# Optimization experiments

Measured on AMD Instinct MI355X. Metric: run time of the kernel, lower is better.

## Reference

```python
import jax, jax.numpy as jnp
import numpy as np

B, L, D_MODEL = 4, 4096, 1024
D_STATE, D_CONV, N_HEADS, CHUNK = 16, 4, 8, 64
D_INNER = 2048
HEADDIM = D_INNER // N_HEADS
CONV_DIM = D_INNER + 2 * D_STATE
D_PROJ = 2 * D_INNER + 2 * D_STATE + N_HEADS
EPS = 1e-5


def _silu(v):
    return v * jax.nn.sigmoid(v)


def _segsum(x):
    # x: (..., T) -> (..., T, T); segsum[i,j] = sum_{j<d<=i} x[d], -inf above diag
    T = x.shape[-1]
    xe = jnp.broadcast_to(x[..., None], (*x.shape, T))
    lower_strict = jnp.tril(jnp.ones((T, T), bool), -1)
    s = jnp.cumsum(jnp.where(lower_strict, xe, 0.0), axis=-2)
    lower = jnp.tril(jnp.ones((T, T), bool), 0)
    return jnp.where(lower, s, -jnp.inf)


def _ssd(x, A, Bm, Cm, chunk):
    # x: (b,l,h,p), A: (b,l,h), Bm/Cm: (b,l,n) (single B/C shared across heads)
    b, l, h, p = x.shape
    n = Bm.shape[-1]
    c = l // chunk
    x = x.reshape(b, c, chunk, h, p)
    A = A.reshape(b, c, chunk, h).transpose(0, 3, 1, 2)  # b h c l
    Bc = Bm.reshape(b, c, chunk, n)
    Cc = Cm.reshape(b, c, chunk, n)
    A_cs = jnp.cumsum(A, axis=-1)                        # b h c l
    Lmat = jnp.exp(_segsum(A))                           # b h c l s
    Y_diag = jnp.einsum('bcln,bcsn,bhcls,bcshp->bclhp', Cc, Bc, Lmat, x)
    decay_states = jnp.exp(A_cs[..., -1:] - A_cs)        # b h c l
    states = jnp.einsum('bcln,bhcl,bclhp->bchpn', Bc, decay_states, x)
    states = jnp.concatenate([jnp.zeros_like(states[:, :1]), states], axis=1)
    A_last = jnp.pad(A_cs[..., -1], ((0, 0), (0, 0), (1, 0)))  # b h (c+1)
    decay_chunk = jnp.exp(_segsum(A_last))               # b h (c+1) (c+1)
    new_states = jnp.einsum('bhzc,bchpn->bzhpn', decay_chunk, states)
    states_prev, final_state = new_states[:, :-1], new_states[:, -1]
    Y_off = jnp.einsum('bcln,bchpn,bhcl->bclhp', Cc, states_prev, jnp.exp(A_cs))
    Y = (Y_diag + Y_off).reshape(b, l, h, p)
    return Y, final_state


def setup_inputs() -> dict:
    key = jax.random.key(0)
    ks = jax.random.split(key, 8)
    inp = {
        'input_tensor': jax.random.normal(ks[0], (B, L, D_MODEL), dtype=jnp.float32),
        'W_in': jax.random.normal(ks[1], (D_PROJ, D_MODEL), dtype=jnp.float32) / np.sqrt(D_MODEL),
        'conv_w': jax.random.normal(ks[2], (CONV_DIM, 1, D_CONV), dtype=jnp.float32) * 0.2,
        'conv_b': jax.random.normal(ks[3], (CONV_DIM,), dtype=jnp.float32) * 0.02,
        'dt_bias': jax.random.uniform(ks[4], (N_HEADS,), dtype=jnp.float32) * 0.1,
        'log_A': jnp.log(jnp.arange(1, N_HEADS + 1, dtype=jnp.float32)),
        'D_skip': jnp.ones((N_HEADS,), dtype=jnp.float32),
        'norm_w': jnp.ones((D_INNER,), dtype=jnp.float32),
        'W_out': jax.random.normal(ks[5], (D_MODEL, D_INNER), dtype=jnp.float32) / np.sqrt(D_INNER),
    }
    return inp


def reference(input_tensor, W_in, conv_w, conv_b, dt_bias, log_A, D_skip, norm_w, W_out):
    bsz, slen, _ = input_tensor.shape
    proj = input_tensor @ W_in.T  # (b,l,D_PROJ)
    z = proj[..., :D_INNER]
    xBC = proj[..., D_INNER:D_INNER + CONV_DIM]
    dt = jax.nn.softplus(proj[..., D_INNER + CONV_DIM:] + dt_bias)  # (b,l,h)
    # causal depthwise conv1d (torch pads both sides then slices [:, :slen])
    xt = jnp.transpose(xBC, (0, 2, 1))  # (b,d,l)
    conv = jax.lax.conv_general_dilated(
        xt, conv_w, window_strides=(1,), padding=[(D_CONV - 1, 0)],
        feature_group_count=CONV_DIM) + conv_b[None, :, None]
    xBC = _silu(jnp.transpose(conv, (0, 2, 1)))
    x = xBC[..., :D_INNER]
    Bm = xBC[..., D_INNER:D_INNER + D_STATE]
    Cm = xBC[..., D_INNER + D_STATE:]
    A = jnp.broadcast_to((-jnp.exp(log_A))[None, None, :], (bsz, slen, N_HEADS))
    xh = x.reshape(bsz, slen, N_HEADS, HEADDIM) * dt[..., None]
    Y, _ = _ssd(xh, A, Bm, Cm, CHUNK)
    Y = Y + xh * D_skip[:, None]
    y = Y.reshape(bsz, slen, D_INNER)
    # gated RMSNorm
    y = y * _silu(z)
    y = y * jax.lax.rsqrt(jnp.mean(y * y, axis=-1, keepdims=True) + EPS) * norm_w
    return y @ W_out.T
```

## Files before the change

kernel.cpp:

```cpp
#include <hip/hip_runtime.h>
#include <hip/hip_bf16.h>
#include <math.h>

#define BATCH   4
#define SEQLEN  4096
#define DMODEL  1024
#define DSTATE  16
#define DCONV   4
#define NHEADS  8
#define CHUNKSZ 64
#define DINNER  2048
#define HEADDIM 256
#define CONVDIM 2080
#define DPROJ   4136
#define NPAD1   4224
#define LDP     4224
#define ROWS    (BATCH*SEQLEN)
#define NCHUNK  (SEQLEN/CHUNKSZ)

typedef unsigned short bf16_t;
typedef __attribute__((ext_vector_type(8))) short bfrag;
typedef __attribute__((ext_vector_type(4))) float f32x4;

__device__ __forceinline__ float sigmoidf_(float v) { return 1.0f / (1.0f + __expf(-v)); }
__device__ __forceinline__ float siluf_(float v)    { return v * sigmoidf_(v); }
__device__ __forceinline__ float softplusf_(float v) {
    return fmaxf(v, 0.f) + log1pf(__expf(-fabsf(v)));
}

__device__ __forceinline__ float bf2f(bf16_t u) {
    union { unsigned int i; float f; } v; v.i = ((unsigned int)u) << 16; return v.f;
}
__device__ __forceinline__ float bflo(unsigned int u) {
    union { unsigned int i; float f; } v; v.i = u << 16; return v.f;
}
__device__ __forceinline__ float bfhi(unsigned int u) {
    union { unsigned int i; float f; } v; v.i = u & 0xffff0000u; return v.f;
}
__device__ __forceinline__ bf16_t f2bf(float f) {
    unsigned int x = __float_as_uint(f);
    unsigned int r = (x + 0x7fffu + ((x >> 16) & 1u)) >> 16;
    return (bf16_t)r;
}
__device__ __forceinline__ unsigned int pack2(float a, float b) {
    return (unsigned int)f2bf(a) | ((unsigned int)f2bf(b) << 16);
}

__device__ __forceinline__ void async_copy16(const bf16_t* g, bf16_t* l) {
    __builtin_amdgcn_global_load_lds(
        (const __attribute__((address_space(1))) void*)g,
        (__attribute__((address_space(3))) void*)l, 16, 0, 0);
}

__global__ __launch_bounds__(256)
void cvt_f32_bf16(const float* __restrict__ src, bf16_t* __restrict__ dst, int n8)
{
    int i = blockIdx.x * 256 + threadIdx.x;
    if (i >= n8) return;
    float4 a = *(const float4*)&src[(size_t)i * 8];
    float4 b = *(const float4*)&src[(size_t)i * 8 + 4];
    uint4 o;
    o.x = pack2(a.x, a.y); o.y = pack2(a.z, a.w);
    o.z = pack2(b.x, b.y); o.w = pack2(b.z, b.w);
    *(uint4*)&dst[(size_t)i * 8] = o;
}

__global__ __launch_bounds__(256)
void cvt_pad_w1(const float* __restrict__ src, bf16_t* __restrict__ dst)
{
    int i = blockIdx.x * 256 + threadIdx.x;
    if (i >= NPAD1 * DMODEL / 4) return;
    size_t e = (size_t)i * 4;
    int row = (int)(e >> 10);
    ushort4 o = make_ushort4(0, 0, 0, 0);
    if (row < DPROJ) {
        float4 v = *(const float4*)&src[e];
        o.x = f2bf(v.x); o.y = f2bf(v.y); o.z = f2bf(v.z); o.w = f2bf(v.w);
    }
    *(ushort4*)&dst[e] = o;
}

__global__ __launch_bounds__(256)
void cvt_w2(const float* __restrict__ W, const float* __restrict__ norm_w,
            bf16_t* __restrict__ dst)
{
    int i = blockIdx.x * 256 + threadIdx.x;
    if (i >= DMODEL * DINNER / 4) return;
    size_t e = (size_t)i * 4;
    int k = (int)(e & (DINNER - 1));
    float4 v = *(const float4*)&W[e];
    float4 w = *(const float4*)&norm_w[k];
    ushort4 o;
    o.x = f2bf(v.x * w.x); o.y = f2bf(v.y * w.y);
    o.z = f2bf(v.z * w.z); o.w = f2bf(v.w * w.w);
    *(ushort4*)&dst[e] = o;
}

template<bool OUT_BF16>
__device__ __forceinline__
void gemm_body(const bf16_t* __restrict__ A, const bf16_t* __restrict__ W,
               void* __restrict__ Cv, const float* __restrict__ rowScale,
               int Nstore, int K, int lda, int ldw, int ldc)
{
    __shared__ __align__(16) bf16_t smem[16384];
    bf16_t* As = smem;
    bf16_t* Ws = smem + 8192;
    const int tid  = threadIdx.x;
    const int wave = tid >> 6, lane = tid & 63;
    const int row0 = blockIdx.y * 128, col0 = blockIdx.x * 128;
    const int wm = (wave >> 1) * 64, wn = (wave & 1) * 64;
    const int quad = lane >> 4, fr = lane & 15;

    const int sr  = lane >> 2;
    const int cph = lane & 3;
    const int r1  = wave * 32 + sr;
    const int cl1 = cph ^ ((r1 >> 1) & 3);
    const bf16_t* gA1 = &A[(size_t)(row0 + r1) * lda + cl1 * 8];
    const bf16_t* gW1 = &W[(size_t)(col0 + r1) * ldw + cl1 * 8];
    const size_t offA16 = (size_t)16 * lda;
    const size_t offW16 = (size_t)16 * ldw;
    const int lo1 = wave * 1024, lo2 = wave * 1024 + 512;

    int aoff[4], boff[4];
    #pragma unroll
    for (int i = 0; i < 4; ++i) {
        int ar = wm + i * 16 + fr;
        aoff[i] = ar * 32 + ((quad ^ ((ar >> 1) & 3)) << 3);
        int br = wn + i * 16 + fr;
        boff[i] = br * 32 + ((quad ^ ((br >> 1) & 3)) << 3);
    }

    f32x4 acc[4][4];
    #pragma unroll
    for (int i = 0; i < 4; ++i)
        #pragma unroll
        for (int j = 0; j < 4; ++j) {
            f32x4 z = {0.f, 0.f, 0.f, 0.f};
            acc[i][j] = z;
        }

    const int niter = K >> 5;
    async_copy16(gA1, &As[lo1]);
    async_copy16(gA1 + offA16, &As[lo2]);
    async_copy16(gW1, &Ws[lo1]);
    async_copy16(gW1 + offW16, &Ws[lo2]);

    for (int it = 0; it < niter; ++it) {
        const int cur = (it & 1) * 4096;
        __syncthreads();
        if (it + 1 < niter) {
            const int nxt = cur ^ 4096;
            const int kt = (it + 1) * 32;
            async_copy16(gA1 + kt, &As[nxt + lo1]);
            async_copy16(gA1 + kt + offA16, &As[nxt + lo2]);
            async_copy16(gW1 + kt, &Ws[nxt + lo1]);
            async_copy16(gW1 + kt + offW16, &Ws[nxt + lo2]);
        }
        bfrag af[4], bfr[4];
        #pragma unroll
        for (int i = 0; i < 4; ++i) af[i]  = *(const bfrag*)&As[cur + aoff[i]];
        #pragma unroll
        for (int j = 0; j < 4; ++j) bfr[j] = *(const bfrag*)&Ws[cur + boff[j]];
        #pragma unroll
        for (int i = 0; i < 4; ++i)
            #pragma unroll
            for (int j = 0; j < 4; ++j)
                acc[i][j] = __builtin_amdgcn_mfma_f32_16x16x32_bf16(
                                af[i], bfr[j], acc[i][j], 0, 0, 0);
    }

    float rs[4][4];
    if (rowScale) {
        #pragma unroll
        for (int i = 0; i < 4; ++i) {
            size_t m = (size_t)row0 + wm + i * 16 + quad * 4;
            #pragma unroll
            for (int r = 0; r < 4; ++r) rs[i][r] = rowScale[m + r];
        }
    } else {
        #pragma unroll
        for (int i = 0; i < 4; ++i)
            #pragma unroll
            for (int r = 0; r < 4; ++r) rs[i][r] = 1.f;
    }

    if (OUT_BF16) {
        __syncthreads();
        bf16_t* C = (bf16_t*)Cv;
        #pragma unroll
        for (int pass = 0; pass < 2; ++pass) {
            if ((wave >> 1) == pass) {
                #pragma unroll
                for (int i = 0; i < 4; ++i)
                    #pragma unroll
                    for (int j = 0; j < 4; ++j) {
                        int col = wn + 16 * j + fr;
                        #pragma unroll
                        for (int r = 0; r < 4; ++r) {
                            int rl = 16 * i + quad * 4 + r;
                            smem[rl * 136 + col] = f2bf(acc[i][j][r] * rs[i][r]);
                        }
                    }
            }
            __syncthreads();
            #pragma unroll
            for (int k = 0; k < 4; ++k) {
                int id = k * 256 + tid;
                int rl = id >> 4, ch = id & 15;
                uint4 v = *(const uint4*)&smem[rl * 136 + ch * 8];
                *(uint4*)&C[(size_t)(row0 + pass * 64 + rl) * ldc + col0 + ch * 8] = v;
            }
            if (pass == 0) __syncthreads();
        }
    } else {
        float* C = (float*)Cv;
        #pragma unroll
        for (int j = 0; j < 4; ++j) {
            int n = col0 + wn + j * 16 + fr;
            if (n < Nstore) {
                #pragma unroll
                for (int i = 0; i < 4; ++i) {
                    size_t m = (size_t)row0 + wm + i * 16 + quad * 4;
                    #pragma unroll
                    for (int r = 0; r < 4; ++r)
                        C[(m + r) * ldc + n] = acc[i][j][r] * rs[i][r];
                }
            }
        }
    }
}

__global__ __launch_bounds__(256)
void gemm_g1(const bf16_t* __restrict__ A, const bf16_t* __restrict__ W,
             void* __restrict__ Cv, const float* __restrict__ rowScale,
             int Nstore, int K, int lda, int ldw, int ldc)
{ gemm_body<true>(A, W, Cv, rowScale, Nstore, K, lda, ldw, ldc); }

__global__ __launch_bounds__(256)
void gemm_g2(const bf16_t* __restrict__ A, const bf16_t* __restrict__ W,
             void* __restrict__ Cv, const float* __restrict__ rowScale,
             int Nstore, int K, int lda, int ldw, int ldc)
{ gemm_body<false>(A, W, Cv, rowScale, Nstore, K, lda, ldw, ldc); }

__global__ __launch_bounds__(256)
void ssd_fused(const bf16_t* __restrict__ proj, const float* __restrict__ conv_w,
               const float* __restrict__ conv_b, const float* __restrict__ dt_bias,
               const float* __restrict__ log_A, const float* __restrict__ D_skip,
               bf16_t* __restrict__ ybuf)
{
    __shared__ float Bc[64][16];
    __shared__ float Cc[64][16];
    __shared__ float Bp[64][16];
    __shared__ float dtc[64];
    __shared__ float dtp[64];
    __shared__ __align__(16) bf16_t sc_b[64][72];
    __shared__ __align__(16) bf16_t xT[256][72];
    __shared__ __align__(16) bf16_t SpT[256][32];
    __shared__ __align__(16) bf16_t A2[64][32];

    const int c = blockIdx.x, h = blockIdx.y, b = blockIdx.z;
    const int t = threadIdx.x;
    const int row0 = b * SEQLEN + c * CHUNKSZ;
    const float a   = -__expf(log_A[h]);
    const float Dsk = D_skip[h];
    const float bias = dt_bias[h];

    {
        int s = t >> 2, ch8 = (t & 3) * 8;
        int l = c * CHUNKSZ + s;
        const bf16_t* base = &proj[(size_t)(row0 + s) * LDP + 4096 + ch8];
        uint4 zz = make_uint4(0, 0, 0, 0);
        uint4 u3 = *(const uint4*)&base[0];
        uint4 u2 = (l >= 1) ? *(const uint4*)&base[-LDP]     : zz;
        uint4 u1 = (l >= 2) ? *(const uint4*)&base[-2 * LDP] : zz;
        uint4 u0 = (l >= 3) ? *(const uint4*)&base[-3 * LDP] : zz;
        float t3[8] = {bflo(u3.x), bfhi(u3.x), bflo(u3.y), bfhi(u3.y),
                       bflo(u3.z), bfhi(u3.z), bflo(u3.w), bfhi(u3.w)};
        float t2[8] = {bflo(u2.x), bfhi(u2.x), bflo(u2.y), bfhi(u2.y),
                       bflo(u2.z), bfhi(u2.z), bflo(u2.w), bfhi(u2.w)};
        float t1[8] = {bflo(u1.x), bfhi(u1.x), bflo(u1.y), bfhi(u1.y),
                       bflo(u1.z), bfhi(u1.z), bflo(u1.w), bfhi(u1.w)};
        float t0[8] = {bflo(u0.x), bfhi(u0.x), bflo(u0.y), bfhi(u0.y),
                       bflo(u0.z), bfhi(u0.z), bflo(u0.w), bfhi(u0.w)};
        #pragma unroll
        for (int j = 0; j < 8; ++j) {
            int ch = ch8 + j;
            float4 w = *(const float4*)&conv_w[(2048 + ch) * 4];
            float av = conv_b[2048 + ch];
            av = fmaf(w.x, t0[j], av);
            av = fmaf(w.y, t1[j], av);
            av = fmaf(w.z, t2[j], av);
            av = fmaf(w.w, t3[j], av);
            float v = siluf_(av);
            if (ch < 16) Bc[s][ch] = v; else Cc[s][ch - 16] = v;
        }
    }
    if (t < 128) {
        int s = t >> 1, ch8 = (t & 1) * 8;
        float vout[8];
        #pragma unroll
        for (int j = 0; j < 8; ++j) vout[j] = 0.f;
        if (c > 0) {
            int l = (c - 1) * CHUNKSZ + s;
            const bf16_t* base = &proj[(size_t)(row0 - CHUNKSZ + s) * LDP + 4096 + ch8];
            uint4 zz = make_uint4(0, 0, 0, 0);
            uint4 u3 = *(const uint4*)&base[0];
            uint4 u2 = (l >= 1) ? *(const uint4*)&base[-LDP]     : zz;
            uint4 u1 = (l >= 2) ? *(const uint4*)&base[-2 * LDP] : zz;
            uint4 u0 = (l >= 3) ? *(const uint4*)&base[-3 * LDP] : zz;
            float t3[8] = {bflo(u3.x), bfhi(u3.x), bflo(u3.y), bfhi(u3.y),
                           bflo(u3.z), bfhi(u3.z), bflo(u3.w), bfhi(u3.w)};
            float t2[8] = {bflo(u2.x), bfhi(u2.x), bflo(u2.y), bfhi(u2.y),
                           bflo(u2.z), bfhi(u2.z), bflo(u2.w), bfhi(u2.w)};
            float t1[8] = {bflo(u1.x), bfhi(u1.x), bflo(u1.y), bfhi(u1.y),
                           bflo(u1.z), bfhi(u1.z), bflo(u1.w), bfhi(u1.w)};
            float t0[8] = {bflo(u0.x), bfhi(u0.x), bflo(u0.y), bfhi(u0.y),
                           bflo(u0.z), bfhi(u0.z), bflo(u0.w), bfhi(u0.w)};
            #pragma unroll
            for (int j = 0; j < 8; ++j) {
                int ch = ch8 + j;
                float4 w = *(const float4*)&conv_w[(2048 + ch) * 4];
                float av = conv_b[2048 + ch];
                av = fmaf(w.x, t0[j], av);
                av = fmaf(w.y, t1[j], av);
                av = fmaf(w.z, t2[j], av);
                av = fmaf(w.w, t3[j], av);
                vout[j] = siluf_(av);
            }
        }
        #pragma unroll
        for (int j = 0; j < 8; ++j) Bp[s][ch8 + j] = vout[j];
    } else if (t < 192) {
        int s = t - 128;
        float v = bf2f(proj[(size_t)(row0 + s) * LDP + 4128 + h]) + bias;
        dtc[s] = softplusf_(v);
    } else {
        int s = t - 192;
        float w = 0.f;
        if (c > 0) {
            float v = bf2f(proj[(size_t)(row0 - CHUNKSZ + s) * LDP + 4128 + h]) + bias;
            w = softplusf_(v) * __expf(a * (float)(63 - s));
        }
        dtp[s] = w;
    }
    __syncthreads();

    {
        int l = t >> 2;
        int sbase = (t & 3) * 16;
        unsigned int pk[8];
        #pragma unroll
        for (int jj = 0; jj < 16; jj += 2) {
            float v0 = 0.f, v1 = 0.f;
            int s0 = sbase + jj, s1 = s0 + 1;
            if (s0 <= l) {
                float dot = 0.f;
                #pragma unroll
                for (int n = 0; n < 16; ++n) dot = fmaf(Cc[l][n], Bc[s0][n], dot);
                v0 = dot * __expf(a * (float)(l - s0));
                if (s0 == l) v0 += Dsk;
            }
            if (s1 <= l) {
                float dot = 0.f;
                #pragma unroll
                for (int n = 0; n < 16; ++n) dot = fmaf(Cc[l][n], Bc[s1][n], dot);
                v1 = dot * __expf(a * (float)(l - s1));
                if (s1 == l) v1 += Dsk;
            }
            pk[jj >> 1] = pack2(v0, v1);
        }
        uint4 u0 = {pk[0], pk[1], pk[2], pk[3]};
        uint4 u1 = {pk[4], pk[5], pk[6], pk[7]};
        *(uint4*)&sc_b[l][sbase]     = u0;
        *(uint4*)&sc_b[l][sbase + 8] = u1;
    }
    if (t < 64) {
        float e = __expf(a * (float)(t + 1));
        unsigned int pk[8];
        #pragma unroll
        for (int n = 0; n < 16; n += 2) pk[n >> 1] = pack2(e * Cc[t][n], e * Cc[t][n + 1]);
        uint4 u0 = {pk[0], pk[1], pk[2], pk[3]};
        uint4 u1 = {pk[4], pk[5], pk[6], pk[7]};
        uint4 zz = make_uint4(0, 0, 0, 0);
        *(uint4*)&A2[t][0]  = u0;
        *(uint4*)&A2[t][8]  = u1;
        *(uint4*)&A2[t][16] = zz;
        *(uint4*)&A2[t][24] = zz;
    }

    {
        const int p = t;
        const int xch = h * HEADDIM + p;
        const float4 w = *(const float4*)&conv_w[(size_t)xch * 4];
        const float cb = conv_b[xch];
        const int colp = 2048 + xch;
        {
            const bf16_t* pr = &proj[(size_t)row0 * LDP + colp];
            int l0 = c * CHUNKSZ;
            float xm3 = (l0 >= 3) ? bf2f(pr[-3 * LDP]) : 0.f;
            float xm2 = (l0 >= 2) ? bf2f(pr[-2 * LDP]) : 0.f;
            float xm1 = (l0 >= 1) ? bf2f(pr[-LDP])     : 0.f;
            #pragma unroll
            for (int s0 = 0; s0 < 64; s0 += 8) {
                float xd[8];
                #pragma unroll
                for (int q = 0; q < 8; ++q) {
                    float xc = bf2f(pr[(size_t)(s0 + q) * LDP]);
                    float av = cb;
                    av = fmaf(w.x, xm3, av);
                    av = fmaf(w.y, xm2, av);
                    av = fmaf(w.z, xm1, av);
                    av = fmaf(w.w, xc, av);
                    xd[q] = siluf_(av) * dtc[s0 + q];
                    xm3 = xm2; xm2 = xm1; xm1 = xc;
                }
                uint4 u;
                u.x = pack2(xd[0], xd[1]); u.y = pack2(xd[2], xd[3]);
                u.z = pack2(xd[4], xd[5]); u.w = pack2(xd[6], xd[7]);
                *(uint4*)&xT[p][s0] = u;
            }
        }
        float Sp[16];
        #pragma unroll
        for (int n = 0; n < 16; ++n) Sp[n] = 0.f;
        if (c > 0) {
            const bf16_t* pr = &proj[(size_t)(row0 - CHUNKSZ) * LDP + colp];
            int l0 = (c - 1) * CHUNKSZ;
            float xm3 = (l0 >= 3) ? bf2f(pr[-3 * LDP]) : 0.f;
            float xm2 = (l0 >= 2) ? bf2f(pr[-2 * LDP]) : 0.f;
            float xm1 = (l0 >= 1) ? bf2f(pr[-LDP])     : 0.f;
            for (int s = 0; s < 64; ++s) {
                float xc = bf2f(pr[(size_t)s * LDP]);
                float av = cb;
                av = fmaf(w.x, xm3, av);
                av = fmaf(w.y, xm2, av);
                av = fmaf(w.z, xm1, av);
                av = fmaf(w.w, xc, av);
                float v = siluf_(av) * dtp[s];
                #pragma unroll
                for (int n = 0; n < 16; ++n) Sp[n] = fmaf(Bp[s][n], v, Sp[n]);
                xm3 = xm2; xm2 = xm1; xm1 = xc;
            }
        }
        unsigned int pk[8];
        #pragma unroll
        for (int n = 0; n < 16; n += 2) pk[n >> 1] = pack2(Sp[n], Sp[n + 1]);
        uint4 u0 = {pk[0], pk[1], pk[2], pk[3]};
        uint4 u1 = {pk[4], pk[5], pk[6], pk[7]};
        uint4 zz = make_uint4(0, 0, 0, 0);
        *(uint4*)&SpT[p][0]  = u0;
        *(uint4*)&SpT[p][8]  = u1;
        *(uint4*)&SpT[p][16] = zz;
        *(uint4*)&SpT[p][24] = zz;
    }
    __syncthreads();

    {
        const int wave = t >> 6, lane = t & 63;
        const int quad = lane >> 4, fr = lane & 15;
        f32x4 acc[4][4];
        #pragma unroll
        for (int i = 0; i < 4; ++i)
            #pragma unroll
            for (int j = 0; j < 4; ++j) {
                f32x4 z = {0.f, 0.f, 0.f, 0.f};
                acc[i][j] = z;
            }
        #pragma unroll
        for (int kk = 0; kk < 2; ++kk) {
            bfrag af[4], bfr[4];
            #pragma unroll
            for (int i = 0; i < 4; ++i)
                af[i] = *(const bfrag*)&sc_b[16 * i + fr][32 * kk + quad * 8];
            #pragma unroll
            for (int j = 0; j < 4; ++j)
                bfr[j] = *(const bfrag*)&xT[64 * wave + 16 * j + fr][32 * kk + quad * 8];
            #pragma unroll
            for (int i = 0; i < 4; ++i)
                #pragma unroll
                for (int j = 0; j < 4; ++j)
                    acc[i][j] = __builtin_amdgcn_mfma_f32_16x16x32_bf16(
                                    af[i], bfr[j], acc[i][j], 0, 0, 0);
        }
        {
            bfrag af[4], bfr[4];
            #pragma unroll
            for (int i = 0; i < 4; ++i)
                af[i] = *(const bfrag*)&A2[16 * i + fr][quad * 8];
            #pragma unroll
            for (int j = 0; j < 4; ++j)
                bfr[j] = *(const bfrag*)&SpT[64 * wave + 16 * j + fr][quad * 8];
            #pragma unroll
            for (int i = 0; i < 4; ++i)
                #pragma unroll
                for (int j = 0; j < 4; ++j)
                    acc[i][j] = __builtin_amdgcn_mfma_f32_16x16x32_bf16(
                                    af[i], bfr[j], acc[i][j], 0, 0, 0);
        }
        __syncthreads();
        bf16_t* buf = &xT[0][0];
        #pragma unroll
        for (int i = 0; i < 4; ++i)
            #pragma unroll
            for (int j = 0; j < 4; ++j) {
                int pc = 64 * wave + 16 * j + fr;
                #pragma unroll
                for (int r = 0; r < 4; ++r) {
                    int l = 16 * i + quad * 4 + r;
                    buf[l * 264 + pc] = f2bf(acc[i][j][r]);
                }
            }
        __syncthreads();
        bf16_t* ybase = &ybuf[(size_t)row0 * DINNER + h * HEADDIM];
        #pragma unroll
        for (int k = 0; k < 8; ++k) {
            int id = k * 256 + t;
            int l = id >> 5, ch = id & 31;
            uint4 v = *(const uint4*)&buf[l * 264 + ch * 8];
            *(uint4*)&ybase[(size_t)l * DINNER + ch * 8] = v;
        }
    }
}

__global__ __launch_bounds__(256)
void gate_kernel(const bf16_t* __restrict__ proj, bf16_t* __restrict__ ybuf,
                 float* __restrict__ rowscale)
{
    __shared__ float red[4];
    int i = blockIdx.x;
    int t = threadIdx.x;
    const bf16_t* zrow = &proj[(size_t)i * LDP];
    bf16_t* yrow = &ybuf[(size_t)i * DINNER];
    uint4 yv = *(const uint4*)&yrow[t * 8];
    uint4 zv = *(const uint4*)&zrow[t * 8];
    float ya[8] = {bflo(yv.x), bfhi(yv.x), bflo(yv.y), bfhi(yv.y),
                   bflo(yv.z), bfhi(yv.z), bflo(yv.w), bfhi(yv.w)};
    float za[8] = {bflo(zv.x), bfhi(zv.x), bflo(zv.y), bfhi(zv.y),
                   bflo(zv.z), bfhi(zv.z), bflo(zv.w), bfhi(zv.w)};
    float g[8];
    float ss = 0.f;
    #pragma unroll
    for (int j = 0; j < 8; ++j) {
        float gv = ya[j] * siluf_(za[j]);
        g[j] = gv;
        ss = fmaf(gv, gv, ss);
    }
    #pragma unroll
    for (int off = 32; off >= 1; off >>= 1) ss += __shfl_down(ss, off);
    if ((t & 63) == 0) red[t >> 6] = ss;
    __syncthreads();
    if (t == 0) {
        float tot = red[0] + red[1] + red[2] + red[3];
        rowscale[i] = rsqrtf(tot / (float)DINNER + 1e-5f);
    }
    uint4 o;
    o.x = pack2(g[0], g[1]); o.y = pack2(g[2], g[3]);
    o.z = pack2(g[4], g[5]); o.w = pack2(g[6], g[7]);
    *(uint4*)&yrow[t * 8] = o;
}

extern "C" void kernel_launch(void* const* d_in, const int* in_sizes, int n_in,
                              void* d_out, int out_size, void* d_ws, size_t ws_size,
                              hipStream_t stream)
{
    const float* input   = (const float*)d_in[0];
    const float* W_in    = (const float*)d_in[1];
    const float* conv_w  = (const float*)d_in[2];
    const float* conv_b  = (const float*)d_in[3];
    const float* dt_bias = (const float*)d_in[4];
    const float* log_A   = (const float*)d_in[5];
    const float* D_skip  = (const float*)d_in[6];
    const float* norm_w  = (const float*)d_in[7];
    const float* W_out   = (const float*)d_in[8];
    float* out = (float*)d_out;

    bf16_t* proj  = (bf16_t*)d_ws;
    bf16_t* region1 = proj + (size_t)ROWS * LDP;
    bf16_t* Wb2   = region1 + (size_t)ROWS * CONVDIM;
    float*  rowscale = (float*)(Wb2 + (size_t)DMODEL * DINNER);
    bf16_t* Ab    = region1;
    bf16_t* Wb1   = Ab + (size_t)ROWS * DMODEL;
    bf16_t* ybuf  = region1;

    size_t need = (size_t)ROWS * LDP * 2 + (size_t)ROWS * CONVDIM * 2
                + (size_t)DMODEL * DINNER * 2 + (size_t)ROWS * 4;
    if (ws_size < need) {
        hipMemsetAsync(d_out, 0, (size_t)out_size * sizeof(float), stream);
        return;
    }

    cvt_f32_bf16<<<(ROWS * DMODEL / 8 + 255) / 256, 256, 0, stream>>>(
        input, Ab, ROWS * DMODEL / 8);
    cvt_pad_w1<<<(NPAD1 * DMODEL / 4 + 255) / 256, 256, 0, stream>>>(W_in, Wb1);
    cvt_w2<<<(DMODEL * DINNER / 4 + 255) / 256, 256, 0, stream>>>(W_out, norm_w, Wb2);

    dim3 g1(NPAD1 / 128, ROWS / 128);
    gemm_g1<<<g1, 256, 0, stream>>>(Ab, Wb1, proj, nullptr,
                                    NPAD1, DMODEL, DMODEL, DMODEL, LDP);
    dim3 gs(NCHUNK, NHEADS, BATCH);
    ssd_fused<<<gs, 256, 0, stream>>>(proj, conv_w, conv_b, dt_bias,
                                      log_A, D_skip, ybuf);
    gate_kernel<<<ROWS, 256, 0, stream>>>(proj, ybuf, rowscale);
    dim3 g2(DMODEL / 128, ROWS / 128);
    gemm_g2<<<g2, 256, 0, stream>>>(ybuf, Wb2, out, rowscale,
                                    DMODEL, DINNER, DINNER, DINNER, DMODEL);
}
```

Baseline: 581.7 us.

## Rewrite bf16 GEMMs with 256x256 tiles, 512 threads and finer-grained async pipeline

```diff
diff --git a/kernel.cpp b/kernel.cpp
--- a/kernel.cpp
+++ b/kernel.cpp
@@ -13,7 +13,7 @@
 #define HEADDIM 256
 #define CONVDIM 2080
 #define DPROJ   4136
-#define NPAD1   4224
+#define NPADW   4352
 #define LDP     4224
 #define ROWS    (BATCH*SEQLEN)
 #define NCHUNK  (SEQLEN/CHUNKSZ)
@@ -50,6 +50,15 @@
     __builtin_amdgcn_global_load_lds(
         (const __attribute__((address_space(1))) void*)g,
         (__attribute__((address_space(3))) void*)l, 16, 0, 0);
+}
+
+template<int N>
+__device__ __forceinline__ void wait_vmcnt() {
+    __builtin_amdgcn_s_waitcnt(0x0F70 | N);
+}
+__device__ __forceinline__ void barrier_() {
+    __builtin_amdgcn_s_barrier();
+    asm volatile("" ::: "memory");
 }
 
 __global__ __launch_bounds__(256)
@@ -69,7 +78,7 @@
 void cvt_pad_w1(const float* __restrict__ src, bf16_t* __restrict__ dst)
 {
     int i = blockIdx.x * 256 + threadIdx.x;
-    if (i >= NPAD1 * DMODEL / 4) return;
+    if (i >= NPADW * DMODEL / 4) return;
     size_t e = (size_t)i * 4;
     int row = (int)(e >> 10);
     ushort4 o = make_ushort4(0, 0, 0, 0);
@@ -96,130 +105,182 @@
     *(ushort4*)&dst[e] = o;
 }
 
+__device__ __forceinline__
+void ld_afrags(bfrag (&af)[4][2], const bf16_t* base, int wmqi, int fr, int quad)
+{
+    #pragma unroll
+    for (int i2 = 0; i2 < 4; ++i2)
+        #pragma unroll
+        for (int kk = 0; kk < 2; ++kk)
+            af[i2][kk] = *(const bfrag*)
+                &base[(wmqi + i2*16 + fr)*64 + (((kk*4 + quad) ^ (fr & 7)) * 8)];
+}
+__device__ __forceinline__
+void ld_bfrags(bfrag (&bf_)[2][2], const bf16_t* base, int wnqj, int fr, int quad)
+{
+    #pragma unroll
+    for (int j2 = 0; j2 < 2; ++j2)
+        #pragma unroll
+        for (int kk = 0; kk < 2; ++kk)
+            bf_[j2][kk] = *(const bfrag*)
+                &base[(wnqj + j2*16 + fr)*64 + (((kk*4 + quad) ^ (fr & 7)) * 8)];
+}
+template<int QI, int QJ>
+__device__ __forceinline__
+void mm8(f32x4 (&acc)[8][4], const bfrag (&af)[4][2], const bfrag (&bf_)[2][2])
+{
+    __builtin_amdgcn_s_setprio(1);
+    #pragma unroll
+    for (int i2 = 0; i2 < 4; ++i2)
+        #pragma unroll
+        for (int j2 = 0; j2 < 2; ++j2)
+            #pragma unroll
+            for (int kk = 0; kk < 2; ++kk)
+                acc[QI*4 + i2][QJ*2 + j2] = __builtin_amdgcn_mfma_f32_16x16x32_bf16(
+                    af[i2][kk], bf_[j2][kk], acc[QI*4 + i2][QJ*2 + j2], 0, 0, 0);
+    __builtin_amdgcn_s_setprio(0);
+}
+
 template<bool OUT_BF16>
 __device__ __forceinline__
-void gemm_body(const bf16_t* __restrict__ A, const bf16_t* __restrict__ W,
-               void* __restrict__ Cv, const float* __restrict__ rowScale,
-               int Nstore, int K, int lda, int ldw, int ldc)
-{
-    __shared__ __align__(16) bf16_t smem[16384];
+void gemm256_body(const bf16_t* __restrict__ A, const bf16_t* __restrict__ W,
+                  void* __restrict__ Cv, const float* __restrict__ rowScale,
+                  int Nstore, int K, int lda, int ldw, int ldc)
+{
+    __shared__ __align__(16) bf16_t smem[65536];
     bf16_t* As = smem;
-    bf16_t* Ws = smem + 8192;
+    bf16_t* Ws = smem + 32768;
+
     const int tid  = threadIdx.x;
     const int wave = tid >> 6, lane = tid & 63;
-    const int row0 = blockIdx.y * 128, col0 = blockIdx.x * 128;
-    const int wm = (wave >> 1) * 64, wn = (wave & 1) * 64;
     const int quad = lane >> 4, fr = lane & 15;
-
-    const int sr  = lane >> 2;
-    const int cph = lane & 3;
-    const int r1  = wave * 32 + sr;
-    const int cl1 = cph ^ ((r1 >> 1) & 3);
-    const bf16_t* gA1 = &A[(size_t)(row0 + r1) * lda + cl1 * 8];
-    const bf16_t* gW1 = &W[(size_t)(col0 + r1) * ldw + cl1 * 8];
-    const size_t offA16 = (size_t)16 * lda;
-    const size_t offW16 = (size_t)16 * ldw;
-    const int lo1 = wave * 1024, lo2 = wave * 1024 + 512;
-
-    int aoff[4], boff[4];
+    const int ln3  = lane >> 3;
+    const int cswz = ((lane & 7) ^ ln3) * 8;
+
+    const int gx   = gridDim.x;
+    const int nwg  = gx * gridDim.y;
+    const int flat = blockIdx.y * gx + blockIdx.x;
+    const int q8   = nwg >> 3;
+    const int swz  = (flat & 7) * q8 + (flat >> 3);
+    const int col0 = (swz % gx) * 256;
+    const int row0 = (swz / gx) * 256;
+
+    const int wm = (wave >> 2) * 128, wn = (wave & 3) * 64;
+
+    const bf16_t* gA[2][2];
+    const bf16_t* gW[2][2];
     #pragma unroll
-    for (int i = 0; i < 4; ++i) {
-        int ar = wm + i * 16 + fr;
-        aoff[i] = ar * 32 + ((quad ^ ((ar >> 1) & 3)) << 3);
-        int br = wn + i * 16 + fr;
-        boff[i] = br * 32 + ((quad ^ ((br >> 1) & 3)) << 3);
-    }
-
-    f32x4 acc[4][4];
+    for (int h = 0; h < 2; ++h)
+        #pragma unroll
+        for (int q = 0; q < 2; ++q) {
+            int rA = 128*q + 8*wave + 64*h;
+            int rB = 128*q + 64*(wave >> 2) + 8*(wave & 3) + 32*h;
+            gA[h][q] = A + (size_t)(row0 + rA + ln3) * lda + cswz;
+            gW[h][q] = W + (size_t)(col0 + rB + ln3) * ldw + cswz;
+        }
+
+#define STG_A(H, Q, NB, K0S)                                                     \
+    async_copy16(gA[H][Q] + (K0S),                                               \
+                 &As[(NB)*16384 + (128*(Q) + 8*wave + 64*(H))*64])
+#define STG_B(H, Q, NB, K0S)                                                     \
+    async_copy16(gW[H][Q] + (K0S),                                               \
+                 &Ws[(NB)*16384 + (128*(Q) + 64*(wave>>2) + 8*(wave&3) + 32*(H))*64])
+
+    f32x4 acc[8][4];
     #pragma unroll
-    for (int i = 0; i < 4; ++i)
+    for (int i = 0; i < 8; ++i)
         #pragma unroll
         for (int j = 0; j < 4; ++j) {
             f32x4 z = {0.f, 0.f, 0.f, 0.f};
             acc[i][j] = z;
         }
-
-    const int niter = K >> 5;
-    async_copy16(gA1, &As[lo1]);
-    async_copy16(gA1 + offA16, &As[lo2]);
-    async_copy16(gW1, &Ws[lo1]);
-    async_copy16(gW1 + offW16, &Ws[lo2]);
-
-    for (int it = 0; it < niter; ++it) {
-        const int cur = (it & 1) * 4096;
-        __syncthreads();
-        if (it + 1 < niter) {
-            const int nxt = cur ^ 4096;
-            const int kt = (it + 1) * 32;
-            async_copy16(gA1 + kt, &As[nxt + lo1]);
-            async_copy16(gA1 + kt + offA16, &As[nxt + lo2]);
-            async_copy16(gW1 + kt, &Ws[nxt + lo1]);
-            async_copy16(gW1 + kt + offW16, &Ws[nxt + lo2]);
-        }
-        bfrag af[4], bfr[4];
-        #pragma unroll
-        for (int i = 0; i < 4; ++i) af[i]  = *(const bfrag*)&As[cur + aoff[i]];
-        #pragma unroll
-        for (int j = 0; j < 4; ++j) bfr[j] = *(const bfrag*)&Ws[cur + boff[j]];
-        #pragma unroll
-        for (int i = 0; i < 4; ++i)
-            #pragma unroll
-            for (int j = 0; j < 4; ++j)
-                acc[i][j] = __builtin_amdgcn_mfma_f32_16x16x32_bf16(
-                                af[i], bfr[j], acc[i][j], 0, 0, 0);
-    }
-
-    float rs[4][4];
-    if (rowScale) {
-        #pragma unroll
-        for (int i = 0; i < 4; ++i) {
-            size_t m = (size_t)row0 + wm + i * 16 + quad * 4;
-            #pragma unroll
-            for (int r = 0; r < 4; ++r) rs[i][r] = rowScale[m + r];
-        }
-    } else {
-        #pragma unroll
-        for (int i = 0; i < 4; ++i)
-            #pragma unroll
-            for (int r = 0; r < 4; ++r) rs[i][r] = 1.f;
-    }
+    bfrag af[4][2], bf_[2][2];
+
+    STG_A(0,0,0,0); STG_A(0,1,0,0);
+    STG_B(0,0,0,0); STG_B(0,1,0,0);
+    STG_B(1,0,0,0); STG_B(1,1,0,0);
+    STG_A(1,0,0,0); STG_A(1,1,0,0);
+
+#define TILE_STEP(BUF_, NB_, K0S_, STG_, V1_, V2_) do {                          \
+          \
+    wait_vmcnt<4>(); barrier_();                                                 \
+    ld_afrags(af, &As[(BUF_)*16384], wm, fr, quad);                              \
+    ld_bfrags(bf_, &Ws[(BUF_)*16384], wn, fr, quad);                             \
+    if (STG_) { STG_A(0,0,NB_,K0S_); STG_A(0,1,NB_,K0S_); }                      \
+    mm8<0,0>(acc, af, bf_);                                                      \
+                                                     \
+    wait_vmcnt<V1_>(); barrier_();                                               \
+    ld_bfrags(bf_, &Ws[(BUF_)*16384], wn + 32, fr, quad);                        \
+    if (STG_) { STG_B(0,0,NB_,K0S_); STG_B(0,1,NB_,K0S_); }                      \
+    mm8<0,1>(acc, af, bf_);                                                      \
+                                                     \
+    wait_vmcnt<V2_>(); barrier_();                                               \
+    ld_afrags(af, &As[(BUF_)*16384], wm + 64, fr, quad);                         \
+    if (STG_) { STG_B(1,0,NB_,K0S_); STG_B(1,1,NB_,K0S_); }                      \
+    mm8<1,1>(acc, af, bf_);                                                      \
+                                     \
+    barrier_();                                                                  \
+    ld_bfrags(bf_, &Ws[(BUF_)*16384], wn, fr, quad);                             \
+    if (STG_) { STG_A(1,0,NB_,K0S_); STG_A(1,1,NB_,K0S_); }                      \
+    mm8<1,0>(acc, af, bf_);                                                      \
+} while (0)
+
+    const int nt = K >> 6;
+    for (int t = 0; t < nt - 1; ++t) {
+        TILE_STEP((t & 1), ((t & 1) ^ 1), ((t + 1) * 64), true, 4, 4);
+    }
+    TILE_STEP(((nt - 1) & 1), 0, 0, false, 2, 0);
+
+#undef TILE_STEP
+#undef STG_A
+#undef STG_B
 
     if (OUT_BF16) {
         __syncthreads();
         bf16_t* C = (bf16_t*)Cv;
         #pragma unroll
         for (int pass = 0; pass < 2; ++pass) {
-            if ((wave >> 1) == pass) {
-                #pragma unroll
-                for (int i = 0; i < 4; ++i)
+            if ((wave >> 2) == pass) {
+                #pragma unroll
+                for (int i = 0; i < 8; ++i)
                     #pragma unroll
                     for (int j = 0; j < 4; ++j) {
                         int col = wn + 16 * j + fr;
                         #pragma unroll
                         for (int r = 0; r < 4; ++r) {
                             int rl = 16 * i + quad * 4 + r;
-                            smem[rl * 136 + col] = f2bf(acc[i][j][r] * rs[i][r]);
+                            smem[rl * 264 + col] = f2bf(acc[i][j][r]);
                         }
                     }
             }
             __syncthreads();
             #pragma unroll
-            for (int k = 0; k < 4; ++k) {
-                int id = k * 256 + tid;
-                int rl = id >> 4, ch = id & 15;
-                uint4 v = *(const uint4*)&smem[rl * 136 + ch * 8];
-                *(uint4*)&C[(size_t)(row0 + pass * 64 + rl) * ldc + col0 + ch * 8] = v;
+            for (int k = 0; k < 8; ++k) {
+                int id = k * 512 + tid;
+                int rl = id >> 5, ch = id & 31;
+                if (col0 + ch * 8 < Nstore) {
+                    uint4 v = *(const uint4*)&smem[rl * 264 + ch * 8];
+                    *(uint4*)&C[(size_t)(row0 + pass * 128 + rl) * ldc
+                                + col0 + ch * 8] = v;
+                }
             }
             if (pass == 0) __syncthreads();
         }
     } else {
+        float rs[8][4];
+        #pragma unroll
+        for (int i = 0; i < 8; ++i) {
+            size_t m = (size_t)row0 + wm + i * 16 + quad * 4;
+            #pragma unroll
+            for (int r = 0; r < 4; ++r) rs[i][r] = rowScale ? rowScale[m + r] : 1.f;
+        }
         float* C = (float*)Cv;
         #pragma unroll
         for (int j = 0; j < 4; ++j) {
             int n = col0 + wn + j * 16 + fr;
             if (n < Nstore) {
                 #pragma unroll
-                for (int i = 0; i < 4; ++i) {
+                for (int i = 0; i < 8; ++i) {
                     size_t m = (size_t)row0 + wm + i * 16 + quad * 4;
                     #pragma unroll
                     for (int r = 0; r < 4; ++r)
@@ -230,17 +291,17 @@
     }
 }
 
-__global__ __launch_bounds__(256)
+__global__ __launch_bounds__(512, 2)
 void gemm_g1(const bf16_t* __restrict__ A, const bf16_t* __restrict__ W,
              void* __restrict__ Cv, const float* __restrict__ rowScale,
              int Nstore, int K, int lda, int ldw, int ldc)
-{ gemm_body<true>(A, W, Cv, rowScale, Nstore, K, lda, ldw, ldc); }
-
-__global__ __launch_bounds__(256)
+{ gemm256_body<true>(A, W, Cv, rowScale, Nstore, K, lda, ldw, ldc); }
+
+__global__ __launch_bounds__(512, 2)
 void gemm_g2(const bf16_t* __restrict__ A, const bf16_t* __restrict__ W,
              void* __restrict__ Cv, const float* __restrict__ rowScale,
              int Nstore, int K, int lda, int ldw, int ldc)
-{ gemm_body<false>(A, W, Cv, rowScale, Nstore, K, lda, ldw, ldc); }
+{ gemm256_body<false>(A, W, Cv, rowScale, Nstore, K, lda, ldw, ldc); }
 
 __global__ __launch_bounds__(256)
 void ssd_fused(const bf16_t* __restrict__ proj, const float* __restrict__ conv_w,
@@ -591,17 +652,17 @@
 
     cvt_f32_bf16<<<(ROWS * DMODEL / 8 + 255) / 256, 256, 0, stream>>>(
         input, Ab, ROWS * DMODEL / 8);
-    cvt_pad_w1<<<(NPAD1 * DMODEL / 4 + 255) / 256, 256, 0, stream>>>(W_in, Wb1);
+    cvt_pad_w1<<<(NPADW * DMODEL / 4 + 255) / 256, 256, 0, stream>>>(W_in, Wb1);
     cvt_w2<<<(DMODEL * DINNER / 4 + 255) / 256, 256, 0, stream>>>(W_out, norm_w, Wb2);
 
-    dim3 g1(NPAD1 / 128, ROWS / 128);
-    gemm_g1<<<g1, 256, 0, stream>>>(Ab, Wb1, proj, nullptr,
-                                    NPAD1, DMODEL, DMODEL, DMODEL, LDP);
+    dim3 g1(NPADW / 256, ROWS / 256);
+    gemm_g1<<<g1, 512, 0, stream>>>(Ab, Wb1, proj, nullptr,
+                                    LDP, DMODEL, DMODEL, DMODEL, LDP);
     dim3 gs(NCHUNK, NHEADS, BATCH);
     ssd_fused<<<gs, 256, 0, stream>>>(proj, conv_w, conv_b, dt_bias,
                                       log_A, D_skip, ybuf);
     gate_kernel<<<ROWS, 256, 0, stream>>>(proj, ybuf, rowscale);
-    dim3 g2(DMODEL / 128, ROWS / 128);
-    gemm_g2<<<g2, 256, 0, stream>>>(ybuf, Wb2, out, rowscale,
+    dim3 g2(DMODEL / 256, ROWS / 256);
+    gemm_g2<<<g2, 512, 0, stream>>>(ybuf, Wb2, out, rowscale,
                                     DMODEL, DINNER, DINNER, DINNER, DMODEL);
 }
```

Result: faster. 533.3 us (-8.3%).
